# Performance work log

Hardware: AMD Instinct MI355X
Metric: run time of the kernel (lower is better)

The kernel has to match this reference:

```python
import jax, jax.numpy as jnp
import numpy as np

A = 9          # num anchors per location
C = 256        # feature channels
H = W = 32     # feature map size
B = 1          # batch (module's squeeze_-based NMS implies batch=1)
N = A * H * W  # total proposals
IOU_THR = 0.9
EPS = 1e-5     # BatchNorm eps
NEG_SLOPE = 0.01  # LeakyReLU default


def setup_inputs() -> dict:
    key = jax.random.key(0)
    ks = jax.random.split(key, 8)
    inp = {
        "x": jax.random.normal(ks[0], (B, C, H, W), dtype=jnp.float32),
        "anchors": jax.random.uniform(ks[1], (A, 4), dtype=jnp.float32),
        # depthwise 3x3 conv (groups=C): torch weight shape [C,1,3,3]
        "dw_w": jax.random.normal(ks[2], (C, 1, 3, 3), dtype=jnp.float32) * 0.05,
        # pointwise 1x1 conv [C_out, C_in]
        "pw_w": jax.random.normal(ks[3], (C, C), dtype=jnp.float32) * 0.05,
        "bn1_gamma": jnp.ones((C,), jnp.float32),
        "bn1_beta": jnp.zeros((C,), jnp.float32),
        "bn1_mean": jnp.zeros((C,), jnp.float32),
        "bn1_var": jnp.ones((C,), jnp.float32),
        # anchors_conv: 1x1 conv 256 -> 4A, BN, ReLU6
        "anc_w": jax.random.normal(ks[4], (4 * A, C), dtype=jnp.float32) * 0.05,
        "anc_gamma": jnp.ones((4 * A,), jnp.float32),
        "anc_beta": jnp.zeros((4 * A,), jnp.float32),
        "anc_mean": jnp.zeros((4 * A,), jnp.float32),
        "anc_var": jnp.ones((4 * A,), jnp.float32),
        # objectness_conv: 1x1 conv 256 -> A, BN, Sigmoid
        "obj_w": jax.random.normal(ks[5], (A, C), dtype=jnp.float32) * 0.05,
        "obj_gamma": jnp.ones((A,), jnp.float32),
        "obj_beta": jnp.zeros((A,), jnp.float32),
        "obj_mean": jnp.zeros((A,), jnp.float32),
        "obj_var": jnp.ones((A,), jnp.float32),
    }
    return inp


def _bn(h, gamma, beta, mean, var):
    # inference-mode BatchNorm2d over channel dim 1 of [B,C,H,W]
    inv = jax.lax.rsqrt(var + EPS)
    return (h - mean[None, :, None, None]) * (inv * gamma)[None, :, None, None] + beta[None, :, None, None]


def _nms_keep(boxes, scores, thr):
    # greedy NMS (torchvision semantics, boxes as x1,y1,x2,y2) -> bool keep mask in original order
    order = jnp.argsort(-scores)
    b = boxes[order]  # [N,4] sorted by score desc
    x1, y1, x2, y2 = b[:, 0], b[:, 1], b[:, 2], b[:, 3]
    areas = (x2 - x1) * (y2 - y1)
    ix1 = jnp.maximum(x1[:, None], x1[None, :])
    iy1 = jnp.maximum(y1[:, None], y1[None, :])
    ix2 = jnp.minimum(x2[:, None], x2[None, :])
    iy2 = jnp.minimum(y2[:, None], y2[None, :])
    inter = jnp.clip(ix2 - ix1, 0.0) * jnp.clip(iy2 - iy1, 0.0)
    iou = inter / (areas[:, None] + areas[None, :] - inter)
    idx = jnp.arange(boxes.shape[0])

    def body(i, keep):
        sup = (iou[i] > thr) & (idx > i) & keep[i]
        return keep & ~sup

    keep_sorted = jax.lax.fori_loop(0, boxes.shape[0], body, jnp.ones((boxes.shape[0],), bool))
    return jnp.zeros((boxes.shape[0],), bool).at[order].set(keep_sorted)


def reference(x, anchors, dw_w, pw_w, bn1_gamma, bn1_beta, bn1_mean, bn1_var,
              anc_w, anc_gamma, anc_beta, anc_mean, anc_var,
              obj_w, obj_gamma, obj_beta, obj_mean, obj_var):
    batch = x.shape[0]
    hw = x.shape[2] * x.shape[3]
    # DepthSeparableConv2d: depthwise 3x3 (groups=C) + pointwise 1x1
    h = jax.lax.conv_general_dilated(
        x, dw_w, window_strides=(1, 1), padding=((1, 1), (1, 1)),
        dimension_numbers=("NCHW", "OIHW", "NCHW"), feature_group_count=C)
    h = jnp.einsum("bchw,oc->bohw", h, pw_w)
    h = jax.nn.leaky_relu(_bn(h, bn1_gamma, bn1_beta, bn1_mean, bn1_var), NEG_SLOPE)
    # heads
    anc = jnp.einsum("bchw,oc->bohw", h, anc_w)
    anc = jnp.clip(_bn(anc, anc_gamma, anc_beta, anc_mean, anc_var), 0.0, 6.0)  # ReLU6
    obj = jnp.einsum("bchw,oc->bohw", h, obj_w)
    obj = jax.nn.sigmoid(_bn(obj, obj_gamma, obj_beta, obj_mean, obj_var))
    # anchor decode
    corr = anc.reshape(batch, A, 4, hw)              # [B,A,4,HW]
    anch = anchors.reshape(1, A, 4, 1)
    pos = corr[:, :, :2, :] + anch[:, :, :2, :]
    size = jnp.exp(corr[:, :, 2:, :]) * anch[:, :, 2:, :]
    corrected = jnp.concatenate([pos, size], axis=2)  # [B,A,4,HW]
    boxes = corrected.transpose(0, 2, 1, 3).reshape(batch, 4, -1).transpose(0, 2, 1)  # [B,N,4]
    scores = obj.reshape(batch, A, 1, hw).transpose(0, 2, 1, 3).reshape(batch, 1, -1).transpose(0, 2, 1)  # [B,N,1]
    boxes = boxes[0]          # squeeze_ (batch==1)
    scores = scores[0, :, 0]
    keep = _nms_keep(boxes, scores, IOU_THR)
    m = jax.lax.stop_gradient(keep.astype(boxes.dtype))
    # fixed-shape equivalent of index_select: suppressed rows zeroed
    return jnp.concatenate([boxes * m[:, None], (scores * m)[:, None]], axis=1)  # [N,5]
```

## Files before the change

### kernel.cpp

```cpp
#include <hip/hip_runtime.h>
#include <hip/hip_bf16.h>

#define EPSF 1e-5f
#define IOU_THRF 0.9f
#define NBOX 9216
#define NWORDS 144
#define CAND_CAP 4096
#define FIRE_CAP 1024
#define NTILES 666

__global__ __launch_bounds__(256) void dw_conv(const float* __restrict__ x,
                                               const float* __restrict__ w,
                                               float* __restrict__ h0) {
    int idx = blockIdx.x * 256 + threadIdx.x;
    int c = idx >> 10, p = idx & 1023;
    int yy = p >> 5, xx = p & 31;
    const float* xi = x + (c << 10);
    const float* wc = w + c * 9;
    float acc = 0.f;
    #pragma unroll
    for (int dy = -1; dy <= 1; ++dy) {
        int y2 = yy + dy;
        if ((unsigned)y2 >= 32u) continue;
        #pragma unroll
        for (int dx = -1; dx <= 1; ++dx) {
            int x2 = xx + dx;
            if ((unsigned)x2 >= 32u) continue;
            acc += wc[(dy + 1) * 3 + (dx + 1)] * xi[y2 * 32 + x2];
        }
    }
    h0[idx] = acc;
}

__global__ __launch_bounds__(256) void pw_conv(const float* __restrict__ h0,
                                               const float* __restrict__ w,
                                               const float* __restrict__ g,
                                               const float* __restrict__ b,
                                               const float* __restrict__ mu,
                                               const float* __restrict__ var,
                                               float* __restrict__ h1) {
    int p = blockIdx.x * 256 + threadIdx.x;
    int o0 = blockIdx.y * 4;
    float acc0 = 0.f, acc1 = 0.f, acc2 = 0.f, acc3 = 0.f;
    for (int c = 0; c < 256; ++c) {
        float hv = h0[(c << 10) + p];
        acc0 += w[(o0 + 0) * 256 + c] * hv;
        acc1 += w[(o0 + 1) * 256 + c] * hv;
        acc2 += w[(o0 + 2) * 256 + c] * hv;
        acc3 += w[(o0 + 3) * 256 + c] * hv;
    }
    float accs[4] = {acc0, acc1, acc2, acc3};
    #pragma unroll
    for (int k = 0; k < 4; ++k) {
        int o = o0 + k;
        float inv = 1.0f / sqrtf(var[o] + EPSF);
        float v = (accs[k] - mu[o]) * (inv * g[o]) + b[o];
        v = (v >= 0.f) ? v : 0.01f * v;
        h1[(o << 10) + p] = v;
    }
}

__global__ __launch_bounds__(256) void heads(const float* __restrict__ h1,
                                             const float* __restrict__ anc_w,
                                             const float* __restrict__ ag,
                                             const float* __restrict__ ab,
                                             const float* __restrict__ am,
                                             const float* __restrict__ av,
                                             const float* __restrict__ obj_w,
                                             const float* __restrict__ og,
                                             const float* __restrict__ ob,
                                             const float* __restrict__ om,
                                             const float* __restrict__ ov,
                                             const float* __restrict__ anchors,
                                             float* __restrict__ boxes,
                                             float* __restrict__ scores) {
    int p = blockIdx.x * 256 + threadIdx.x;
    int o = blockIdx.y;
    const float* wrow = (o < 36) ? (anc_w + o * 256) : (obj_w + (o - 36) * 256);
    float acc = 0.f;
    for (int c = 0; c < 256; ++c) acc += wrow[c] * h1[(c << 10) + p];
    if (o < 36) {
        float inv = 1.0f / sqrtf(av[o] + EPSF);
        float v = (acc - am[o]) * (inv * ag[o]) + ab[o];
        v = fminf(fmaxf(v, 0.f), 6.f);
        int a = o >> 2, k = o & 3;
        float anch = anchors[a * 4 + k];
        float val = (k < 2) ? (v + anch) : (expf(v) * anch);
        boxes[(size_t)(a * 1024 + p) * 4 + k] = val;
    } else {
        int a = o - 36;
        float inv = 1.0f / sqrtf(ov[a] + EPSF);
        float v = (acc - om[a]) * (inv * og[a]) + ob[a];
        scores[a * 1024 + p] = 1.0f / (1.0f + expf(-v));
    }
}

__global__ __launch_bounds__(256) void rank_partial(const float* __restrict__ scores,
                                                    unsigned* __restrict__ rank) {
    __shared__ float4 sm[144];
    int mbase = blockIdx.y * 576;
    for (int t = threadIdx.x; t < 144; t += 256)
        sm[t] = ((const float4*)(scores + mbase))[t];
    __syncthreads();
    int n = blockIdx.x * 256 + threadIdx.x;
    float s = scores[n];
    unsigned cnt = 0;
    for (int q = 0; q < 144; ++q) {
        float4 v = sm[q];
        int m = mbase + q * 4;
        cnt += (v.x > s) || (v.x == s && (m + 0) < n);
        cnt += (v.y > s) || (v.y == s && (m + 1) < n);
        cnt += (v.z > s) || (v.z == s && (m + 2) < n);
        cnt += (v.w > s) || (v.w == s && (m + 3) < n);
    }
    atomicAdd(&rank[n], cnt);
}

__global__ __launch_bounds__(256) void scatter_sorted(const float* __restrict__ boxes,
                                                      const unsigned* __restrict__ rank,
                                                      int* __restrict__ order,
                                                      float* __restrict__ sboxes,
                                                      float* __restrict__ sareas) {
    int n = blockIdx.x * 256 + threadIdx.x;
    unsigned r = rank[n];
    order[r] = n;
    float4 bx = ((const float4*)boxes)[n];
    ((float4*)sboxes)[r] = bx;
    sareas[r] = (bx.z - bx.x) * (bx.w - bx.y);
}

__global__ __launch_bounds__(256) void cand_detect(const float* __restrict__ sboxes,
                                                   const float* __restrict__ sareas,
                                                   unsigned long long* __restrict__ rnz64) {
    __shared__ float CX1[256], CY1[256], CX2[256], CY2[256], CAR[256];
    int rem = blockIdx.x, rb = 0;
    while (rem >= 36 - rb) { rem -= 36 - rb; ++rb; }
    int s = rb + rem;
    int tid = threadIdx.x;
    int i = rb * 256 + tid;
    {
        int j = s * 256 + tid;
        float4 cb = ((const float4*)sboxes)[j];
        CX1[tid] = cb.x; CY1[tid] = cb.y; CX2[tid] = cb.z; CY2[tid] = cb.w;
        CAR[tid] = sareas[j];
    }
    __syncthreads();
    float4 b = ((const float4*)sboxes)[i];
    float ar = sareas[i];
    bool any = false;

    if (s == rb) {
        for (int idx = tid + 1; idx < 256; ++idx) {
            float ix = fminf(b.z, CX2[idx]) - fmaxf(b.x, CX1[idx]);
            float iy = fminf(b.w, CY2[idx]) - fmaxf(b.y, CY1[idx]);
            float inter = fmaxf(ix, 0.f) * fmaxf(iy, 0.f);
            float denom = ar + CAR[idx] - inter;
            if (inter > 0.85f * denom) {
                if (inter / denom > IOU_THRF) any = true;
            }
        }
    } else {
        const float4* X1v = (const float4*)CX1;
        const float4* Y1v = (const float4*)CY1;
        const float4* X2v = (const float4*)CX2;
        const float4* Y2v = (const float4*)CY2;
        const float4* ARv = (const float4*)CAR;
        #pragma unroll 2
        for (int q = 0; q < 64; ++q) {
            float4 x1 = X1v[q], y1 = Y1v[q], x2 = X2v[q], y2 = Y2v[q], aa = ARv[q];
            #define CCHK(k) { \
                float ix = fminf(b.z, x2.k) - fmaxf(b.x, x1.k); \
                float iy = fminf(b.w, y2.k) - fmaxf(b.y, y1.k); \
                float inter = fmaxf(ix, 0.f) * fmaxf(iy, 0.f);  \
                float denom = ar + aa.k - inter;                \
                if (inter > 0.85f * denom) {                    \
                    if (inter / denom > IOU_THRF) any = true;   \
                } }
            CCHK(x) CCHK(y) CCHK(z) CCHK(w)
            #undef CCHK
        }
    }
    unsigned long long bal = __ballot(any);
    if ((tid & 63) == 0) atomicOr(&rnz64[rb * 4 + (tid >> 6)], bal);
}

__device__ inline unsigned long long rdl64(unsigned long long v, int l) {
    unsigned lo = (unsigned)__builtin_amdgcn_readlane((int)(unsigned)(v & 0xffffffffull), l);
    unsigned hi = (unsigned)__builtin_amdgcn_readlane((int)(unsigned)(v >> 32), l);
    return ((unsigned long long)hi << 32) | lo;
}

__global__ __launch_bounds__(256) void compact_cand2(const unsigned long long* __restrict__ rnz64,
                                                     const float* __restrict__ sboxes,
                                                     const float* __restrict__ sareas,
                                                     int* __restrict__ cidx,
                                                     float4* __restrict__ cboxes,
                                                     float* __restrict__ carea,
                                                     int* __restrict__ knum) {
    __shared__ int incl[256];
    int tid = threadIdx.x;
    int myc = (tid < NWORDS) ? (int)__popcll(rnz64[tid]) : 0;
    incl[tid] = myc;
    __syncthreads();
    #pragma unroll
    for (int offd = 1; offd < 256; offd <<= 1) {
        int v = (tid >= offd) ? incl[tid - offd] : 0;
        __syncthreads();
        incl[tid] += v;
        __syncthreads();
    }
    if (blockIdx.x == 0 && tid == 0) {
        int tot = incl[NWORDS - 1];
        knum[0] = tot < CAND_CAP ? tot : CAND_CAP;
    }
    int i = blockIdx.x * 256 + tid;
    int w = i >> 6, l = i & 63;
    unsigned long long bits = rnz64[w];
    if (bits & (1ull << l)) {
        int base = incl[w] - (int)__popcll(bits);
        int pos = base + (int)__popcll(bits & ((1ull << l) - 1ull));
        if (pos < CAND_CAP) {
            cidx[pos] = i;
            cboxes[pos] = ((const float4*)sboxes)[i];
            carea[pos] = sareas[i];
        }
    }
}

__global__ __launch_bounds__(256) void gate_build(const float4* __restrict__ cboxes,
                                                  const float* __restrict__ carea,
                                                  const int* __restrict__ knum,
                                                  unsigned long long* __restrict__ gate,
                                                  unsigned long long* __restrict__ diag0,
                                                  unsigned long long* __restrict__ diag1) {
    int Kc = knum[0];
    int a = blockIdx.x * 4 + (threadIdx.x >> 6);
    int w = threadIdx.x & 63;
    if (a >= Kc) return;
    float4 b = cboxes[a];
    float ar = carea[a];
    unsigned long long bits = 0ull;
    int cbase = w * 64;
    if (cbase < Kc) {
        int lim = Kc - cbase; if (lim > 64) lim = 64;
        for (int t = 0; t < lim; ++t) {
            int c = cbase + t;
            if (c > a) {
                float4 cb = cboxes[c];
                float ix = fminf(b.z, cb.z) - fmaxf(b.x, cb.x);
                float iy = fminf(b.w, cb.w) - fmaxf(b.y, cb.y);
                float inter = fmaxf(ix, 0.f) * fmaxf(iy, 0.f);
                float denom = ar + carea[c] - inter;
                if (inter > 0.85f * denom) {
                    if (inter / denom > IOU_THRF) bits |= (1ull << t);
                }
            }
        }
    }
    gate[(size_t)a * 64 + w] = bits;
    int aw = a >> 6;
    if (w == aw) diag0[a] = bits;
    if (w == aw + 1) diag1[a] = bits;
}

__global__ __launch_bounds__(512) void nms_scan5(const unsigned long long* __restrict__ gate,
                                                 const unsigned long long* __restrict__ diag0,
                                                 const unsigned long long* __restrict__ diag1,
                                                 const int* __restrict__ knum,
                                                 int* __restrict__ fire_ord,
                                                 int* __restrict__ fire_cnt) {
    __shared__ unsigned long long d0L[CAND_CAP];
    __shared__ unsigned long long d1L[CAND_CAP];
    __shared__ unsigned long long supL[64];
    __shared__ int flist[2][64];
    __shared__ int fcnt[2];
    int tid = threadIdx.x;
    int Kc = knum[0];
    int nw = (Kc + 63) >> 6;

    #pragma unroll
    for (int q = 0; q < CAND_CAP / 512; ++q) {
        d0L[tid + 512 * q] = diag0[tid + 512 * q];
        d1L[tid + 512 * q] = diag1[tid + 512 * q];
    }
    if (tid < 64) supL[tid] = 0ull;
    if (tid == 0) { fcnt[0] = 0; fcnt[1] = 0; }
    __syncthreads();

    int nf = 0;
    unsigned long long carry = 0ull;

    for (int w = 0; w < nw; ++w) {
        if (tid >= 64) {
            int wv = (tid >> 6) - 1;
            int j = tid & 63;
            int fp = fcnt[(w + 1) & 1];
            for (int f = wv; f < fp; f += 7) {
                int o = flist[(w + 1) & 1][f];
                if (j < nw) {
                    unsigned long long g = gate[(size_t)o * 64 + j];
                    if (g) atomicOr(&supL[j], g);
                }
            }
        } else {
            int rem = Kc - (w << 6);
            unsigned long long maskw = (rem >= 64) ? ~0ull : ((1ull << rem) - 1ull);
            unsigned long long alive = ~(supL[w] | carry) & maskw;
            unsigned long long carry_next = 0ull;
            int myf = 0;
            while (alive) {
                int t = __builtin_ctzll(alive);
                int o = (w << 6) + t;
                if (tid == 0) {
                    if (nf < FIRE_CAP) fire_ord[nf] = o;
                    flist[w & 1][myf] = o;
                }
                ++nf; ++myf;
                unsigned long long dd0 = d0L[o];
                unsigned long long dd1 = d1L[o];
                alive &= ~(1ull << t);
                alive &= ~dd0;
                carry_next |= dd1;
            }
            if (tid == 0) fcnt[w & 1] = myf;
            carry = carry_next;
        }
        __syncthreads();
    }
    if (tid == 0) fire_cnt[0] = nf < FIRE_CAP ? nf : FIRE_CAP;
}

__global__ __launch_bounds__(256) void finalize(const float* __restrict__ sboxes,
                                                const float* __restrict__ sareas,
                                                const float* __restrict__ scores,
                                                const int* __restrict__ order,
                                                const float4* __restrict__ cboxes,
                                                const float* __restrict__ carea,
                                                const int* __restrict__ cidx,
                                                const int* __restrict__ fire_ord,
                                                const int* __restrict__ fire_cnt,
                                                float* __restrict__ out) {
    __shared__ float4 FB[FIRE_CAP];
    __shared__ float FA[FIRE_CAP];
    __shared__ int FP[FIRE_CAP];
    int tid = threadIdx.x;
    int fc = fire_cnt[0];
    for (int k = tid; k < fc; k += 256) {
        int o = fire_ord[k];
        FB[k] = cboxes[o];
        FA[k] = carea[o];
        FP[k] = cidx[o];
    }
    __syncthreads();
    int j = blockIdx.x * 256 + tid;
    float4 b = ((const float4*)sboxes)[j];
    float aj = sareas[j];
    bool supp = false;
    for (int k = 0; k < fc; ++k) {
        float4 f = FB[k];
        float ix = fminf(b.z, f.z) - fmaxf(b.x, f.x);
        float iy = fminf(b.w, f.w) - fmaxf(b.y, f.y);
        float inter = fmaxf(ix, 0.f) * fmaxf(iy, 0.f);
        float denom = FA[k] + aj - inter;
        if (FP[k] < j && inter > 0.85f * denom) {
            if (inter / denom > IOU_THRF) supp = true;
        }
    }
    int n = order[j];
    float m = supp ? 0.f : 1.f;
    out[(size_t)n * 5 + 0] = b.x * m;
    out[(size_t)n * 5 + 1] = b.y * m;
    out[(size_t)n * 5 + 2] = b.z * m;
    out[(size_t)n * 5 + 3] = b.w * m;
    out[(size_t)n * 5 + 4] = scores[n] * m;
}

extern "C" void kernel_launch(void* const* d_in, const int* in_sizes, int n_in,
                              void* d_out, int out_size, void* d_ws, size_t ws_size,
                              hipStream_t stream) {
    const float* x      = (const float*)d_in[0];
    const float* anchors= (const float*)d_in[1];
    const float* dw_w   = (const float*)d_in[2];
    const float* pw_w   = (const float*)d_in[3];
    const float* bn1g   = (const float*)d_in[4];
    const float* bn1b   = (const float*)d_in[5];
    const float* bn1m   = (const float*)d_in[6];
    const float* bn1v   = (const float*)d_in[7];
    const float* anc_w  = (const float*)d_in[8];
    const float* ag     = (const float*)d_in[9];
    const float* ab     = (const float*)d_in[10];
    const float* am     = (const float*)d_in[11];
    const float* av     = (const float*)d_in[12];
    const float* obj_w  = (const float*)d_in[13];
    const float* og     = (const float*)d_in[14];
    const float* ob     = (const float*)d_in[15];
    const float* om     = (const float*)d_in[16];
    const float* ov     = (const float*)d_in[17];
    float* out = (float*)d_out;

    char* ws = (char*)d_ws;
    size_t off = 0;
    auto alloc = [&](size_t bytes) -> char* {
        char* p = ws + off;
        off = (off + bytes + 255) & ~(size_t)255;
        return p;
    };
    float* h0      = (float*)alloc(256 * 1024 * 4);
    float* h1      = (float*)alloc(256 * 1024 * 4);
    float* boxes   = (float*)alloc(NBOX * 4 * 4);
    float* scores  = (float*)alloc(NBOX * 4);
    unsigned* rank = (unsigned*)alloc(NBOX * 4);
    int* order     = (int*)alloc(NBOX * 4);
    float* sboxes  = (float*)alloc(NBOX * 4 * 4);
    float* sareas  = (float*)alloc(NBOX * 4);
    unsigned long long* rnz64 = (unsigned long long*)alloc(192 * 8);
    int* cidx      = (int*)alloc(CAND_CAP * 4);
    float4* cboxes = (float4*)alloc(CAND_CAP * 16);
    float* carea   = (float*)alloc(CAND_CAP * 4);
    int* knum      = (int*)alloc(256);
    int* fire_ord  = (int*)alloc(FIRE_CAP * 4);
    int* fire_cnt  = (int*)alloc(256);
    unsigned long long* gate  = (unsigned long long*)alloc((size_t)CAND_CAP * 64 * 8);
    unsigned long long* diag0 = (unsigned long long*)alloc(CAND_CAP * 8);
    unsigned long long* diag1 = (unsigned long long*)alloc(CAND_CAP * 8);

    hipMemsetAsync(rank, 0, NBOX * 4, stream);
    hipMemsetAsync(rnz64, 0, 192 * 8, stream);

    dw_conv<<<1024, 256, 0, stream>>>(x, dw_w, h0);
    pw_conv<<<dim3(4, 64), 256, 0, stream>>>(h0, pw_w, bn1g, bn1b, bn1m, bn1v, h1);
    heads<<<dim3(4, 45), 256, 0, stream>>>(h1, anc_w, ag, ab, am, av,
                                           obj_w, og, ob, om, ov, anchors, boxes, scores);
    rank_partial<<<dim3(36, 16), 256, 0, stream>>>(scores, rank);
    scatter_sorted<<<36, 256, 0, stream>>>(boxes, rank, order, sboxes, sareas);
    cand_detect<<<NTILES, 256, 0, stream>>>(sboxes, sareas, rnz64);
    compact_cand2<<<36, 256, 0, stream>>>(rnz64, sboxes, sareas, cidx, cboxes, carea, knum);
    gate_build<<<CAND_CAP / 4, 256, 0, stream>>>(cboxes, carea, knum, gate, diag0, diag1);
    nms_scan5<<<1, 512, 0, stream>>>(gate, diag0, diag1, knum, fire_ord, fire_cnt);
    finalize<<<36, 256, 0, stream>>>(sboxes, sareas, scores, order,
                                     cboxes, carea, cidx, fire_ord, fire_cnt, out);
}
```

Measured before the change: 316.7 us.

## Restructure candidate detection into 512x128 tiles with a cheap prefilter

The candidate-detection kernel now gives each thread two row boxes against a 128-column tile staged as float4 in shared memory, instead of one row box against a 256-column tile. A division-free necessary condition (inter > 0.85/1.85*(area_i+area_j)) is OR-accumulated in the main loop. The exact IoU check runs only for threads whose prefilter fired. This raises per-thread work and data reuse and removes branches from the hot loop, at the cost of a second pass over the tile for flagged rows and a changed tile count.

```diff
diff --git a/kernel.cpp b/kernel.cpp
--- a/kernel.cpp
+++ b/kernel.cpp
@@ -7,7 +7,7 @@
 #define NWORDS 144
 #define CAND_CAP 4096
 #define FIRE_CAP 1024
-#define NTILES 666
+#define CD_TILES 684
 
 __global__ __launch_bounds__(256) void dw_conv(const float* __restrict__ x,
                                                const float* __restrict__ w,
@@ -132,56 +132,80 @@
 __global__ __launch_bounds__(256) void cand_detect(const float* __restrict__ sboxes,
                                                    const float* __restrict__ sareas,
                                                    unsigned long long* __restrict__ rnz64) {
-    __shared__ float CX1[256], CY1[256], CX2[256], CY2[256], CAR[256];
-    int rem = blockIdx.x, rb = 0;
-    while (rem >= 36 - rb) { rem -= 36 - rb; ++rb; }
-    int s = rb + rem;
+    __shared__ float4 B4[128];
+    __shared__ float CARs[128];
+    int rem = blockIdx.x, rg = 0;
+    while (rem >= 72 - 4 * rg) { rem -= 72 - 4 * rg; ++rg; }
+    int sc = 4 * rg + rem;
     int tid = threadIdx.x;
-    int i = rb * 256 + tid;
-    {
-        int j = s * 256 + tid;
-        float4 cb = ((const float4*)sboxes)[j];
-        CX1[tid] = cb.x; CY1[tid] = cb.y; CX2[tid] = cb.z; CY2[tid] = cb.w;
-        CAR[tid] = sareas[j];
+    const float SC = 0.85f / 1.85f;
+    if (tid < 128) {
+        int j = sc * 128 + tid;
+        B4[tid] = ((const float4*)sboxes)[j];
+        CARs[tid] = sareas[j];
     }
     __syncthreads();
-    float4 b = ((const float4*)sboxes)[i];
-    float ar = sareas[i];
-    bool any = false;
-
-    if (s == rb) {
-        for (int idx = tid + 1; idx < 256; ++idx) {
-            float ix = fminf(b.z, CX2[idx]) - fmaxf(b.x, CX1[idx]);
-            float iy = fminf(b.w, CY2[idx]) - fmaxf(b.y, CY1[idx]);
+    int i0 = rg * 512 + tid, i1 = i0 + 256;
+    float4 bb0 = ((const float4*)sboxes)[i0];
+    float4 bb1 = ((const float4*)sboxes)[i1];
+    float ar0 = sareas[i0], ar1 = sareas[i1];
+    bool p0 = false, p1 = false;
+
+    if (sc >= 4 * rg + 4) {
+        #pragma unroll 4
+        for (int idx = 0; idx < 128; ++idx) {
+            float4 cb = B4[idx]; float aa = CARs[idx];
+            float ix0 = fminf(bb0.z, cb.z) - fmaxf(bb0.x, cb.x);
+            float iy0 = fminf(bb0.w, cb.w) - fmaxf(bb0.y, cb.y);
+            float t0 = fmaxf(ix0, 0.f) * fmaxf(iy0, 0.f);
+            p0 |= t0 > SC * (ar0 + aa);
+            float ix1 = fminf(bb1.z, cb.z) - fmaxf(bb1.x, cb.x);
+            float iy1 = fminf(bb1.w, cb.w) - fmaxf(bb1.y, cb.y);
+            float t1 = fmaxf(ix1, 0.f) * fmaxf(iy1, 0.f);
+            p1 |= t1 > SC * (ar1 + aa);
+        }
+    } else {
+        #pragma unroll 4
+        for (int idx = 0; idx < 128; ++idx) {
+            int j = sc * 128 + idx;
+            float4 cb = B4[idx]; float aa = CARs[idx];
+            float ix0 = fminf(bb0.z, cb.z) - fmaxf(bb0.x, cb.x);
+            float iy0 = fminf(bb0.w, cb.w) - fmaxf(bb0.y, cb.y);
+            float t0 = fmaxf(ix0, 0.f) * fmaxf(iy0, 0.f);
+            p0 |= (j > i0) && (t0 > SC * (ar0 + aa));
+            float ix1 = fminf(bb1.z, cb.z) - fmaxf(bb1.x, cb.x);
+            float iy1 = fminf(bb1.w, cb.w) - fmaxf(bb1.y, cb.y);
+            float t1 = fmaxf(ix1, 0.f) * fmaxf(iy1, 0.f);
+            p1 |= (j > i1) && (t1 > SC * (ar1 + aa));
+        }
+    }
+    bool cand0 = false, cand1 = false;
+    if (p0) {
+        for (int idx = 0; idx < 128; ++idx) {
+            float4 cb = B4[idx];
+            float ix = fminf(bb0.z, cb.z) - fmaxf(bb0.x, cb.x);
+            float iy = fminf(bb0.w, cb.w) - fmaxf(bb0.y, cb.y);
             float inter = fmaxf(ix, 0.f) * fmaxf(iy, 0.f);
-            float denom = ar + CAR[idx] - inter;
-            if (inter > 0.85f * denom) {
-                if (inter / denom > IOU_THRF) any = true;
-            }
-        }
-    } else {
-        const float4* X1v = (const float4*)CX1;
-        const float4* Y1v = (const float4*)CY1;
-        const float4* X2v = (const float4*)CX2;
-        const float4* Y2v = (const float4*)CY2;
-        const float4* ARv = (const float4*)CAR;
-        #pragma unroll 2
-        for (int q = 0; q < 64; ++q) {
-            float4 x1 = X1v[q], y1 = Y1v[q], x2 = X2v[q], y2 = Y2v[q], aa = ARv[q];
-            #define CCHK(k) { \
-                float ix = fminf(b.z, x2.k) - fmaxf(b.x, x1.k); \
-                float iy = fminf(b.w, y2.k) - fmaxf(b.y, y1.k); \
-                float inter = fmaxf(ix, 0.f) * fmaxf(iy, 0.f);  \
-                float denom = ar + aa.k - inter;                \
-                if (inter > 0.85f * denom) {                    \
-                    if (inter / denom > IOU_THRF) any = true;   \
-                } }
-            CCHK(x) CCHK(y) CCHK(z) CCHK(w)
-            #undef CCHK
-        }
-    }
-    unsigned long long bal = __ballot(any);
-    if ((tid & 63) == 0) atomicOr(&rnz64[rb * 4 + (tid >> 6)], bal);
+            float denom = ar0 + CARs[idx] - inter;
+            int j = sc * 128 + idx;
+            if (j > i0 && inter / denom > IOU_THRF) cand0 = true;
+        }
+    }
+    if (p1) {
+        for (int idx = 0; idx < 128; ++idx) {
+            float4 cb = B4[idx];
+            float ix = fminf(bb1.z, cb.z) - fmaxf(bb1.x, cb.x);
+            float iy = fminf(bb1.w, cb.w) - fmaxf(bb1.y, cb.y);
+            float inter = fmaxf(ix, 0.f) * fmaxf(iy, 0.f);
+            float denom = ar1 + CARs[idx] - inter;
+            int j = sc * 128 + idx;
+            if (j > i1 && inter / denom > IOU_THRF) cand1 = true;
+        }
+    }
+    unsigned long long bal = __ballot(cand0);
+    if ((tid & 63) == 0) atomicOr(&rnz64[rg * 8 + (tid >> 6)], bal);
+    bal = __ballot(cand1);
+    if ((tid & 63) == 0) atomicOr(&rnz64[rg * 8 + 4 + (tid >> 6)], bal);
 }
 
 __device__ inline unsigned long long rdl64(unsigned long long v, int l) {
@@ -433,7 +457,7 @@
                                            obj_w, og, ob, om, ov, anchors, boxes, scores);
     rank_partial<<<dim3(36, 16), 256, 0, stream>>>(scores, rank);
     scatter_sorted<<<36, 256, 0, stream>>>(boxes, rank, order, sboxes, sareas);
-    cand_detect<<<NTILES, 256, 0, stream>>>(sboxes, sareas, rnz64);
+    cand_detect<<<CD_TILES, 256, 0, stream>>>(sboxes, sareas, rnz64);
     compact_cand2<<<36, 256, 0, stream>>>(rnz64, sboxes, sareas, cidx, cboxes, carea, knum);
     gate_build<<<CAND_CAP / 4, 256, 0, stream>>>(cboxes, carea, knum, gate, diag0, diag1);
     nms_scan5<<<1, 512, 0, stream>>>(gate, diag0, diag1, knum, fire_ord, fire_cnt);
```

Measured after the change: 335.1 us. 5.8% more time.
